# Optimization experiments

Measured on AMD Instinct MI355X. Metric: run time of the kernel, lower is better.

Reference implementation:

```python
import jax, jax.numpy as jnp
import numpy as np

N_NODES = 10000
N_EDGES = 320000
IN_DIM = 256
OUT_DIM = 256
N_REL = 16


def setup_inputs() -> dict:
    key = jax.random.key(0)
    k_x, k_src, k_dst, k_et, k_wr, k_w0 = jax.random.split(key, 6)
    x = jax.random.normal(k_x, (N_NODES, IN_DIM), dtype=jnp.float32)
    src = jax.random.randint(k_src, (N_EDGES,), 0, N_NODES)
    dst = jax.random.randint(k_dst, (N_EDGES,), 0, N_NODES)
    edge_index = jnp.stack([src, dst], axis=0)  # [2, E]
    edge_type = jax.random.randint(k_et, (N_EDGES,), 0, N_REL)
    # Xavier-uniform-ish init for weights
    lim_r = float(np.sqrt(6.0 / (IN_DIM + OUT_DIM)))
    W_r = jax.random.uniform(k_wr, (N_REL, IN_DIM, OUT_DIM), minval=-lim_r, maxval=lim_r, dtype=jnp.float32)
    W0_w = jax.random.uniform(k_w0, (OUT_DIM, IN_DIM), minval=-lim_r, maxval=lim_r, dtype=jnp.float32)
    W0_b = jnp.zeros((OUT_DIM,), dtype=jnp.float32)
    return {
        "x": x,
        "W_r": W_r,
        "W0_w": W0_w,
        "W0_b": W0_b,
        "edge_index": edge_index,
        "edge_type": edge_type,
        "num_nodes_local": N_NODES,
    }


def reference(x, W_r, W0_w, W0_b, edge_index, edge_type, num_nodes_local):
    N = num_nodes_local
    R = W_r.shape[0]
    src = edge_index[0]
    dst = edge_index[1]
    # Per-(relation, dst-node) in-degree, clamped at 1 (matches deg_r.clamp_min(1))
    deg = jnp.zeros((R, N), dtype=x.dtype).at[edge_type, dst].add(1.0)
    deg = jnp.maximum(deg, 1.0)  # [R, N]
    # Transform all nodes under every relation weight: grouped GEMM [R, N, out]
    h_all = jnp.einsum('nd,rdo->rno', x, W_r)
    # Gather per-edge message and normalize by relation-specific dst degree
    msg = h_all[edge_type, src] / deg[edge_type, dst][:, None]  # [E, out]
    # Scatter-add messages to destination nodes
    agg = jax.ops.segment_sum(msg, dst, num_segments=N)  # [N, out]
    # Self-loop transform W_0(x)
    return agg + x @ W0_w.T + W0_b
```

## Files before the change

### kernel.cpp

```cpp
#include <hip/hip_runtime.h>

typedef __bf16 bf16x8 __attribute__((ext_vector_type(8)));
typedef float f32x4 __attribute__((ext_vector_type(4)));

static __device__ __forceinline__ unsigned short f2bf(float f) {
    union { float f; unsigned int u; } v; v.f = f;
    unsigned int r = v.u + 0x7fffu + ((v.u >> 16) & 1u);
    return (unsigned short)(r >> 16);
}
static __device__ __forceinline__ float blo(unsigned int u) {
    union { unsigned int u; float f; } v; v.u = u << 16; return v.f;
}
static __device__ __forceinline__ float bhi(unsigned int u) {
    union { unsigned int u; float f; } v; v.u = u & 0xffff0000u; return v.f;
}
static __device__ __forceinline__ unsigned int pack2(float a, float b) {
    return (unsigned int)f2bf(a) | ((unsigned int)f2bf(b) << 16);
}

__global__ void zero_kernel(int* __restrict__ p, int n) {
    int i = blockIdx.x * blockDim.x + threadIdx.x;
    int n4 = n >> 2;
    if (i < n4) reinterpret_cast<int4*>(p)[i] = make_int4(0, 0, 0, 0);
    if (i < (n & 3)) p[(n4 << 2) + i] = 0;
}

__global__ void prep_kernel(const int* __restrict__ dst, const int* __restrict__ et,
                            int* __restrict__ deg,
                            const float* __restrict__ Wr, const float* __restrict__ W0w,
                            unsigned short* __restrict__ Wt2,
                            const float* __restrict__ x, unsigned short* __restrict__ s,
                            int E, int N, int R, int nh, int nw) {
    const int bid = blockIdx.x, tid = threadIdx.x;
    const int K = (R + 1) * 256;
    if (bid < nh) {
        int i = bid * 256 + tid;
        if (i < E) atomicAdd(&deg[et[i] * N + dst[i]], 1);
    } else if (bid < nh + nw) {
        int t = bid - nh;
        int o = t / (R + 1), kb = t - o * (R + 1);
        float v = (kb < R) ? Wr[(((size_t)kb << 8) + tid) * 256 + o]
                           : W0w[((size_t)o << 8) + tid];
        Wt2[(size_t)o * K + (kb << 8) + tid] = f2bf(v);
    } else {
        int id = (bid - nh - nw) * 256 + tid;
        int n = id >> 6, c4 = id & 63;
        if (n < N) {
            float4 v = *reinterpret_cast<const float4*>(&x[((size_t)n << 8) + (c4 << 2)]);
            ushort4 h;
            h.x = f2bf(v.x); h.y = f2bf(v.y); h.z = f2bf(v.z); h.w = f2bf(v.w);
            *reinterpret_cast<ushort4*>(&s[(size_t)n * K + (K - 256) + (c4 << 2)]) = h;
        }
    }
}

__global__ void scan1_kernel(const int* __restrict__ deg, int* __restrict__ local,
                             int* __restrict__ bsum, int* __restrict__ ctr, int B) {
    __shared__ int tmp[256];
    int t = threadIdx.x, g = blockIdx.x * 256 + t;
    int v = (g < B) ? deg[g] : 0;
    tmp[t] = v; __syncthreads();
    for (int o = 1; o < 256; o <<= 1) {
        int u = (t >= o) ? tmp[t - o] : 0;
        __syncthreads();
        tmp[t] += u;
        __syncthreads();
    }
    if (g < B) { local[g] = tmp[t] - v; ctr[g] = 0; }
    if (t == 255) bsum[blockIdx.x] = tmp[t];
}

__global__ void scan2_kernel(const int* __restrict__ bsum, int* __restrict__ base, int nc) {
    __shared__ int tmp[1024];
    int t = threadIdx.x;
    int v = (t < nc) ? bsum[t] : 0;
    tmp[t] = v; __syncthreads();
    for (int o = 1; o < 1024; o <<= 1) {
        int u = (t >= o) ? tmp[t - o] : 0;
        __syncthreads();
        tmp[t] += u;
        __syncthreads();
    }
    if (t < nc) base[t] = tmp[t] - v;
}

__global__ void scatter_ids_kernel(const int* __restrict__ src, const int* __restrict__ dst,
                                   const int* __restrict__ et, const int* __restrict__ local,
                                   const int* __restrict__ base, int* __restrict__ ctr,
                                   int* __restrict__ srcs, int E, int N) {
    int i = blockIdx.x * blockDim.x + threadIdx.x;
    if (i < E) {
        int b = et[i] * N + dst[i];
        int p = local[b] + base[b >> 8] + atomicAdd(&ctr[b], 1);
        srcs[p] = src[i];
    }
}

__global__ __launch_bounds__(256) void reduce_kernel(
    const int* __restrict__ srcs, const int* __restrict__ deg,
    const int* __restrict__ local, const int* __restrict__ base,
    unsigned short* __restrict__ s, int N, int R)
{
    const int K = (R + 1) * 256;
    const int r = blockIdx.y;
    const int dn = blockIdx.x * 8 + (threadIdx.x >> 5);
    if (dn >= N) return;
    const int lane = threadIdx.x & 31;
    const int bin = r * N + dn;
    const int cnt = deg[bin];
    const int st  = local[bin] + base[bin >> 8];

    float a0 = 0.f, a1 = 0.f, a2 = 0.f, a3 = 0.f;
    float a4 = 0.f, a5 = 0.f, a6 = 0.f, a7 = 0.f;
    for (int c0 = 0; c0 < cnt; c0 += 32) {
        int sv = 0;
        if (c0 + lane < cnt) sv = srcs[st + c0 + lane];
        int m = cnt - c0; if (m > 32) m = 32;
        for (int i = 0; i < m; ++i) {
            int sn = __shfl(sv, i, 32);
            const uint4 v = *reinterpret_cast<const uint4*>(
                &s[(size_t)sn * K + (K - 256) + (lane << 3)]);
            a0 += blo(v.x); a1 += bhi(v.x);
            a2 += blo(v.y); a3 += bhi(v.y);
            a4 += blo(v.z); a5 += bhi(v.z);
            a6 += blo(v.w); a7 += bhi(v.w);
        }
    }
    if (cnt > 0) {
        float sc = 1.0f / (float)cnt;
        a0 *= sc; a1 *= sc; a2 *= sc; a3 *= sc;
        a4 *= sc; a5 *= sc; a6 *= sc; a7 *= sc;
    }
    uint4 o;
    o.x = pack2(a0, a1); o.y = pack2(a2, a3);
    o.z = pack2(a4, a5); o.w = pack2(a6, a7);
    *reinterpret_cast<uint4*>(&s[(size_t)dn * K + (r << 8) + (lane << 3)]) = o;
}

__global__ __launch_bounds__(256) void gemm_kernel(
    const unsigned short* __restrict__ S, const unsigned short* __restrict__ Wt2,
    const float* __restrict__ bias, float* __restrict__ dest,
    int M, int K, int ksteps, int addbias)
{
    __shared__ __align__(16) unsigned short ldsA[2][4096];
    __shared__ __align__(16) unsigned short ldsB[8192];
    const int tid = threadIdx.x;
    const int lane = tid & 63, w = tid >> 6;
    const int wm = w & 1, wn = w >> 1;
    const int m0 = blockIdx.x * 64, n0 = blockIdx.y * 128;
    const int kstart = blockIdx.z * ksteps * 64;
    const size_t rowb = (size_t)K * 2;

    f32x4 acc[2][4] = {};

#define STAGE_A(buf, kstep)                                                               \
    {                                                                                     \
        const int kb = (kstart + (kstep) * 64) * 2;                                       \
        _Pragma("unroll")                                                                 \
        for (int i = 0; i < 2; ++i) {                                                     \
            int flat = (w * 2 + i) * 64 + lane;                                           \
            int row = flat >> 3, seg = flat & 7;                                          \
            int gr = m0 + row; gr = gr < M ? gr : M - 1;                                  \
            const char* gp = (const char*)S + (size_t)gr * rowb + kb                      \
                             + ((seg * 16) ^ ((row & 7) << 4));                           \
            unsigned short* lp = &ldsA[buf][(w * 2 + i) * 512];                           \
            __builtin_amdgcn_global_load_lds(                                             \
                (const __attribute__((address_space(1))) void*)gp,                        \
                (__attribute__((address_space(3))) void*)lp, 16, 0, 0);                   \
        }                                                                                 \
    }

#define STAGE_B(kstep)                                                                    \
    {                                                                                     \
        const int kb = (kstart + (kstep) * 64) * 2;                                       \
        _Pragma("unroll")                                                                 \
        for (int i = 0; i < 4; ++i) {                                                     \
            int flat = (w * 4 + i) * 64 + lane;                                           \
            int row = flat >> 3, seg = flat & 7;                                          \
            const char* gp = (const char*)Wt2 + (size_t)(n0 + row) * rowb + kb            \
                             + ((seg * 16) ^ ((row & 7) << 4));                           \
            unsigned short* lp = &ldsB[(w * 4 + i) * 512];                                \
            __builtin_amdgcn_global_load_lds(                                             \
                (const __attribute__((address_space(1))) void*)gp,                        \
                (__attribute__((address_space(3))) void*)lp, 16, 0, 0);                   \
        }                                                                                 \
    }

#define COMPUTE(buf)                                                                      \
    {                                                                                     \
        _Pragma("unroll")                                                                 \
        for (int kk = 0; kk < 2; ++kk) {                                                  \
            bf16x8 af[2], bfr[4];                                                         \
            _Pragma("unroll")                                                             \
            for (int m = 0; m < 2; ++m) {                                                 \
                int row = wm * 32 + m * 16 + (lane & 15);                                 \
                int colb = (kk * 64 + ((lane >> 4) << 4)) ^ ((row & 7) << 4);             \
                af[m] = *reinterpret_cast<const bf16x8*>(                                 \
                    (const char*)&ldsA[buf][0] + row * 128 + colb);                       \
            }                                                                             \
            _Pragma("unroll")                                                             \
            for (int n = 0; n < 4; ++n) {                                                 \
                int row = wn * 64 + n * 16 + (lane & 15);                                 \
                int colb = (kk * 64 + ((lane >> 4) << 4)) ^ ((row & 7) << 4);             \
                bfr[n] = *reinterpret_cast<const bf16x8*>(                                \
                    (const char*)&ldsB[0] + row * 128 + colb);                            \
            }                                                                             \
            __builtin_amdgcn_s_setprio(1);                                                \
            _Pragma("unroll")                                                             \
            for (int m = 0; m < 2; ++m)                                                   \
                _Pragma("unroll")                                                         \
                for (int n = 0; n < 4; ++n)                                               \
                    acc[m][n] = __builtin_amdgcn_mfma_f32_16x16x32_bf16(                  \
                        af[m], bfr[n], acc[m][n], 0, 0, 0);                               \
            __builtin_amdgcn_s_setprio(0);                                                \
        }                                                                                 \
    }

    STAGE_A(0, 0)
    STAGE_B(0)
    STAGE_A(1, 1)
    asm volatile("s_waitcnt vmcnt(2)" ::: "memory");
    __builtin_amdgcn_s_barrier();

    for (int t = 0; t < ksteps; ++t) {
        COMPUTE(t & 1)
        asm volatile("s_waitcnt lgkmcnt(0)" ::: "memory");
        __builtin_amdgcn_sched_barrier(0);
        __builtin_amdgcn_s_barrier();
        if (t + 1 < ksteps) {
            STAGE_B(t + 1)
            if (t + 2 < ksteps) {
                STAGE_A(t & 1, t + 2)
                asm volatile("s_waitcnt vmcnt(2)" ::: "memory");
            } else {
                asm volatile("s_waitcnt vmcnt(0)" ::: "memory");
            }
            __builtin_amdgcn_s_barrier();
        }
    }
#undef STAGE_A
#undef STAGE_B
#undef COMPUTE

    float* dst = dest + (size_t)blockIdx.z * M * 256;
    const int rbase = m0 + wm * 32 + ((lane >> 4) << 2);
    const int cbase = n0 + wn * 64 + (lane & 15);
    #pragma unroll
    for (int n = 0; n < 4; ++n) {
        int c = cbase + n * 16;
        float bv = addbias ? bias[c] : 0.0f;
        #pragma unroll
        for (int m = 0; m < 2; ++m) {
            #pragma unroll
            for (int j = 0; j < 4; ++j) {
                int r = rbase + m * 16 + j;
                if (r < M) dst[(size_t)r * 256 + c] = acc[m][n][j] + bv;
            }
        }
    }
}

__global__ void combine_kernel(const float* __restrict__ pbuf, const float* __restrict__ bias,
                               float* __restrict__ out, int M, int KZ) {
    int id = blockIdx.x * blockDim.x + threadIdx.x;
    if (id >= M * 64) return;
    int n = id >> 6, c4 = id & 63;
    float4 a = *reinterpret_cast<const float4*>(&pbuf[((size_t)n << 8) + (c4 << 2)]);
    for (int kz = 1; kz < KZ; ++kz) {
        float4 b = *reinterpret_cast<const float4*>(&pbuf[(size_t)kz * M * 256 + ((size_t)n << 8) + (c4 << 2)]);
        a.x += b.x; a.y += b.y; a.z += b.z; a.w += b.w;
    }
    const float4 bv = *reinterpret_cast<const float4*>(&bias[c4 << 2]);
    a.x += bv.x; a.y += bv.y; a.z += bv.z; a.w += bv.w;
    *reinterpret_cast<float4*>(&out[((size_t)n << 8) + (c4 << 2)]) = a;
}

extern "C" void kernel_launch(void* const* d_in, const int* in_sizes, int n_in,
                              void* d_out, int out_size, void* d_ws, size_t ws_size,
                              hipStream_t stream) {
    const float* x   = (const float*)d_in[0];
    const float* Wr  = (const float*)d_in[1];
    const float* W0w = (const float*)d_in[2];
    const float* W0b = (const float*)d_in[3];
    const int*   eidx= (const int*)d_in[4];
    const int*   et  = (const int*)d_in[5];
    const int N = in_sizes[0] / 256;
    const int R = in_sizes[1] / 65536;
    const int E = in_sizes[5];
    const int* src = eidx;
    const int* dst = eidx + E;
    float* out = (float*)d_out;

    const int B = R * N;
    const int NC = (B + 255) / 256;
    const int K = (R + 1) * 256;

    const size_t sz_pslice = (size_t)N * 256 * 4;
    const size_t sz_sort = (((size_t)B * 4 + 255) & ~255UL) * 3
                         + (((size_t)E * 4 + 255) & ~255UL)
                         + 2 * 4096;
    const size_t sz_wt2 = (size_t)256 * K * 2;
    const size_t sz_s   = (size_t)N * K * 2;
    int KZ = 1;
    for (int kz = 4; kz >= 1; kz >>= 1) {
        size_t r0 = (kz > 1) ? (size_t)kz * sz_pslice : 0;
        if (sz_sort > r0) r0 = sz_sort;
        size_t need = ((r0 + 255) & ~255UL) + ((sz_wt2 + 255) & ~255UL) + sz_s + 1024;
        if (need <= ws_size || kz == 1) { KZ = kz; break; }
    }

    char* ws = (char*)d_ws;
    size_t off = 0;
    auto alloc = [&](size_t bytes) { void* p = ws + off; off = (off + bytes + 255) & ~(size_t)255; return p; };
    float* pbuf = (float*)ws;
    int* deg    = (int*)alloc((size_t)B * 4);
    int* local  = (int*)alloc((size_t)B * 4);
    int* bsum   = (int*)alloc(4096);
    int* base   = (int*)alloc(4096);
    int* ctr    = (int*)alloc((size_t)B * 4);
    int* srcs   = (int*)alloc((size_t)E * 4);
    size_t region0 = (KZ > 1) ? (size_t)KZ * sz_pslice : 0;
    if (off > region0) region0 = off;
    off = (region0 + 255) & ~(size_t)255;
    unsigned short* Wt2 = (unsigned short*)alloc(sz_wt2);
    unsigned short* s   = (unsigned short*)alloc(sz_s);

    zero_kernel<<<(B / 4 + 255) / 256, 256, 0, stream>>>(deg, B);
    {
        const int nh = (E + 255) / 256;
        const int nw = (R + 1) * 256;
        const int nx = (N * 64 + 255) / 256;
        prep_kernel<<<nh + nw + nx, 256, 0, stream>>>(dst, et, deg, Wr, W0w, Wt2, x, s,
                                                      E, N, R, nh, nw);
    }
    scan1_kernel<<<NC, 256, 0, stream>>>(deg, local, bsum, ctr, B);
    scan2_kernel<<<1, 1024, 0, stream>>>(bsum, base, NC);
    scatter_ids_kernel<<<(E + 255) / 256, 256, 0, stream>>>(src, dst, et, local, base, ctr, srcs, E, N);
    {
        dim3 g((N + 7) / 8, R);
        reduce_kernel<<<g, 256, 0, stream>>>(srcs, deg, local, base, s, N, R);
    }
    {
        const int ktot = K / 64;
        const int ksteps = ktot / KZ;
        dim3 grid((N + 63) / 64, 2, KZ);
        if (KZ == 1) {
            gemm_kernel<<<grid, 256, 0, stream>>>(s, Wt2, W0b, out, N, K, ksteps, 1);
        } else {
            gemm_kernel<<<grid, 256, 0, stream>>>(s, Wt2, W0b, pbuf, N, K, ksteps, 0);
            combine_kernel<<<(N * 64 + 255) / 256, 256, 0, stream>>>(pbuf, W0b, out, N, KZ);
        }
    }
}
```

Baseline: 141.8 us.

## Fuse per-relation gather-mean into GEMM A-tile staging with fixed 4-way K split

Replaces the separate reduce kernel, which wrote mean-aggregated bf16 rows into a large [N, (R+1)*256] buffer, with a fused kernel. That kernel gathers neighbor features per relation straight into LDS and runs the MFMA GEMM over that relation's 256-wide K slice. A 64x256 output tile per block is accumulated across a fixed split of relations into four partial buffers, which a combine kernel then sums. This removes the round trip of the big intermediate through global memory. In exchange, each block serializes its gather latency before the MFMA work, and the workspace-size check is dropped in favor of always allocating four partial slices.

```diff
diff --git a/kernel.cpp b/kernel.cpp
--- a/kernel.cpp
+++ b/kernel.cpp
@@ -29,7 +29,7 @@
                             int* __restrict__ deg,
                             const float* __restrict__ Wr, const float* __restrict__ W0w,
                             unsigned short* __restrict__ Wt2,
-                            const float* __restrict__ x, unsigned short* __restrict__ s,
+                            const float* __restrict__ x, unsigned short* __restrict__ xbf,
                             int E, int N, int R, int nh, int nw) {
     const int bid = blockIdx.x, tid = threadIdx.x;
     const int K = (R + 1) * 256;
@@ -49,7 +49,7 @@
             float4 v = *reinterpret_cast<const float4*>(&x[((size_t)n << 8) + (c4 << 2)]);
             ushort4 h;
             h.x = f2bf(v.x); h.y = f2bf(v.y); h.z = f2bf(v.z); h.w = f2bf(v.w);
-            *reinterpret_cast<ushort4*>(&s[(size_t)n * K + (K - 256) + (c4 << 2)]) = h;
+            *reinterpret_cast<ushort4*>(&xbf[((size_t)n << 8) + (c4 << 2)]) = h;
         }
     }
 }
@@ -96,165 +96,139 @@
     }
 }
 
-__global__ __launch_bounds__(256) void reduce_kernel(
-    const int* __restrict__ srcs, const int* __restrict__ deg,
-    const int* __restrict__ local, const int* __restrict__ base,
-    unsigned short* __restrict__ s, int N, int R)
+__global__ __launch_bounds__(256) void fused_kernel(
+    const unsigned short* __restrict__ xbf, const unsigned short* __restrict__ Wt2,
+    const int* __restrict__ deg, const int* __restrict__ local,
+    const int* __restrict__ basep, const int* __restrict__ srcs,
+    float* __restrict__ pbuf, int M, int R, int K)
 {
-    const int K = (R + 1) * 256;
-    const int r = blockIdx.y;
-    const int dn = blockIdx.x * 8 + (threadIdx.x >> 5);
-    if (dn >= N) return;
-    const int lane = threadIdx.x & 31;
-    const int bin = r * N + dn;
-    const int cnt = deg[bin];
-    const int st  = local[bin] + base[bin >> 8];
-
-    float a0 = 0.f, a1 = 0.f, a2 = 0.f, a3 = 0.f;
-    float a4 = 0.f, a5 = 0.f, a6 = 0.f, a7 = 0.f;
-    for (int c0 = 0; c0 < cnt; c0 += 32) {
-        int sv = 0;
-        if (c0 + lane < cnt) sv = srcs[st + c0 + lane];
-        int m = cnt - c0; if (m > 32) m = 32;
-        for (int i = 0; i < m; ++i) {
-            int sn = __shfl(sv, i, 32);
-            const uint4 v = *reinterpret_cast<const uint4*>(
-                &s[(size_t)sn * K + (K - 256) + (lane << 3)]);
-            a0 += blo(v.x); a1 += bhi(v.x);
-            a2 += blo(v.y); a3 += bhi(v.y);
-            a4 += blo(v.z); a5 += bhi(v.z);
-            a6 += blo(v.w); a7 += bhi(v.w);
-        }
-    }
-    if (cnt > 0) {
-        float sc = 1.0f / (float)cnt;
-        a0 *= sc; a1 *= sc; a2 *= sc; a3 *= sc;
-        a4 *= sc; a5 *= sc; a6 *= sc; a7 *= sc;
-    }
-    uint4 o;
-    o.x = pack2(a0, a1); o.y = pack2(a2, a3);
-    o.z = pack2(a4, a5); o.w = pack2(a6, a7);
-    *reinterpret_cast<uint4*>(&s[(size_t)dn * K + (r << 8) + (lane << 3)]) = o;
-}
-
-__global__ __launch_bounds__(256) void gemm_kernel(
-    const unsigned short* __restrict__ S, const unsigned short* __restrict__ Wt2,
-    const float* __restrict__ bias, float* __restrict__ dest,
-    int M, int K, int ksteps, int addbias)
-{
-    __shared__ __align__(16) unsigned short ldsA[2][4096];
-    __shared__ __align__(16) unsigned short ldsB[8192];
+    __shared__ __align__(16) unsigned short ldsA[64 * 256];
+    __shared__ __align__(16) unsigned short ldsB[2][256 * 32];
     const int tid = threadIdx.x;
     const int lane = tid & 63, w = tid >> 6;
-    const int wm = w & 1, wn = w >> 1;
-    const int m0 = blockIdx.x * 64, n0 = blockIdx.y * 128;
-    const int kstart = blockIdx.z * ksteps * 64;
-    const size_t rowb = (size_t)K * 2;
-
-    f32x4 acc[2][4] = {};
-
-#define STAGE_A(buf, kstep)                                                               \
+    const int hw = tid >> 5, l = tid & 31;
+    const int m0 = blockIdx.x * 64;
+    const int z = blockIdx.y;
+    const int sl0 = (z * (R + 1)) >> 2, sl1 = ((z + 1) * (R + 1)) >> 2;
+    const size_t rowbW = (size_t)K * 2;
+
+    f32x4 acc[4][4] = {};
+
+#define STAGE_B(buf, sl, ks)                                                              \
     {                                                                                     \
-        const int kb = (kstart + (kstep) * 64) * 2;                                       \
+        const size_t kb = ((size_t)(sl) * 256 + (size_t)(ks) * 32) * 2;                   \
         _Pragma("unroll")                                                                 \
-        for (int i = 0; i < 2; ++i) {                                                     \
-            int flat = (w * 2 + i) * 64 + lane;                                           \
-            int row = flat >> 3, seg = flat & 7;                                          \
-            int gr = m0 + row; gr = gr < M ? gr : M - 1;                                  \
-            const char* gp = (const char*)S + (size_t)gr * rowb + kb                      \
-                             + ((seg * 16) ^ ((row & 7) << 4));                           \
-            unsigned short* lp = &ldsA[buf][(w * 2 + i) * 512];                           \
+        for (int i = 0; i < 4; ++i) {                                                     \
+            int flat = i * 256 + tid;                                                     \
+            int rowq = flat >> 2, seg = flat & 3;                                         \
+            const char* gp = (const char*)Wt2 + (size_t)rowq * rowbW + kb                 \
+                             + ((seg << 4) ^ ((rowq & 3) << 4));                          \
+            unsigned short* lp = &ldsB[buf][flat << 3];                                   \
             __builtin_amdgcn_global_load_lds(                                             \
                 (const __attribute__((address_space(1))) void*)gp,                        \
                 (__attribute__((address_space(3))) void*)lp, 16, 0, 0);                   \
         }                                                                                 \
     }
 
-#define STAGE_B(kstep)                                                                    \
+#define COMPUTE(buf, ks)                                                                  \
     {                                                                                     \
-        const int kb = (kstart + (kstep) * 64) * 2;                                       \
+        bf16x8 af[4], bfr[4];                                                             \
         _Pragma("unroll")                                                                 \
-        for (int i = 0; i < 4; ++i) {                                                     \
-            int flat = (w * 4 + i) * 64 + lane;                                           \
-            int row = flat >> 3, seg = flat & 7;                                          \
-            const char* gp = (const char*)Wt2 + (size_t)(n0 + row) * rowb + kb            \
-                             + ((seg * 16) ^ ((row & 7) << 4));                           \
-            unsigned short* lp = &ldsB[(w * 4 + i) * 512];                                \
-            __builtin_amdgcn_global_load_lds(                                             \
-                (const __attribute__((address_space(1))) void*)gp,                        \
-                (__attribute__((address_space(3))) void*)lp, 16, 0, 0);                   \
+        for (int mi = 0; mi < 4; ++mi) {                                                  \
+            int row = mi * 16 + (lane & 15);                                              \
+            int colb = ((ks) * 64 + ((lane >> 4) << 4)) ^ ((row & 7) << 4);               \
+            af[mi] = *reinterpret_cast<const bf16x8*>((const char*)ldsA + row * 512 + colb); \
         }                                                                                 \
-    }
-
-#define COMPUTE(buf)                                                                      \
-    {                                                                                     \
         _Pragma("unroll")                                                                 \
-        for (int kk = 0; kk < 2; ++kk) {                                                  \
-            bf16x8 af[2], bfr[4];                                                         \
+        for (int ni = 0; ni < 4; ++ni) {                                                  \
+            int row = w * 64 + ni * 16 + (lane & 15);                                     \
+            int colb = (((lane >> 4) << 4)) ^ ((row & 3) << 4);                           \
+            bfr[ni] = *reinterpret_cast<const bf16x8*>((const char*)&ldsB[buf][0] + row * 64 + colb); \
+        }                                                                                 \
+        __builtin_amdgcn_s_setprio(1);                                                    \
+        _Pragma("unroll")                                                                 \
+        for (int mi = 0; mi < 4; ++mi)                                                    \
             _Pragma("unroll")                                                             \
-            for (int m = 0; m < 2; ++m) {                                                 \
-                int row = wm * 32 + m * 16 + (lane & 15);                                 \
-                int colb = (kk * 64 + ((lane >> 4) << 4)) ^ ((row & 7) << 4);             \
-                af[m] = *reinterpret_cast<const bf16x8*>(                                 \
-                    (const char*)&ldsA[buf][0] + row * 128 + colb);                       \
-            }                                                                             \
-            _Pragma("unroll")                                                             \
-            for (int n = 0; n < 4; ++n) {                                                 \
-                int row = wn * 64 + n * 16 + (lane & 15);                                 \
-                int colb = (kk * 64 + ((lane >> 4) << 4)) ^ ((row & 7) << 4);             \
-                bfr[n] = *reinterpret_cast<const bf16x8*>(                                \
-                    (const char*)&ldsB[0] + row * 128 + colb);                            \
-            }                                                                             \
-            __builtin_amdgcn_s_setprio(1);                                                \
-            _Pragma("unroll")                                                             \
-            for (int m = 0; m < 2; ++m)                                                   \
-                _Pragma("unroll")                                                         \
-                for (int n = 0; n < 4; ++n)                                               \
-                    acc[m][n] = __builtin_amdgcn_mfma_f32_16x16x32_bf16(                  \
-                        af[m], bfr[n], acc[m][n], 0, 0, 0);                               \
-            __builtin_amdgcn_s_setprio(0);                                                \
-        }                                                                                 \
-    }
-
-    STAGE_A(0, 0)
-    STAGE_B(0)
-    STAGE_A(1, 1)
-    asm volatile("s_waitcnt vmcnt(2)" ::: "memory");
-    __builtin_amdgcn_s_barrier();
-
-    for (int t = 0; t < ksteps; ++t) {
-        COMPUTE(t & 1)
-        asm volatile("s_waitcnt lgkmcnt(0)" ::: "memory");
+            for (int ni = 0; ni < 4; ++ni)                                                \
+                acc[mi][ni] = __builtin_amdgcn_mfma_f32_16x16x32_bf16(                    \
+                    af[mi], bfr[ni], acc[mi][ni], 0, 0, 0);                               \
+        __builtin_amdgcn_s_setprio(0);                                                    \
+    }
+
+    for (int sl = sl0; sl < sl1; ++sl) {
+        STAGE_B(0, sl, 0)
+        if (sl == R) {
+            #pragma unroll
+            for (int j = 0; j < 8; ++j) {
+                int row = hw * 8 + j;
+                int dn = m0 + row;
+                uint4 v = make_uint4(0, 0, 0, 0);
+                if (dn < M) v = *reinterpret_cast<const uint4*>(&xbf[((size_t)dn << 8) + (l << 3)]);
+                *reinterpret_cast<uint4*>((char*)ldsA + row * 512 + (((l << 4)) ^ ((row & 7) << 4))) = v;
+            }
+        } else {
+            for (int j = 0; j < 8; ++j) {
+                int row = hw * 8 + j;
+                int dn = m0 + row;
+                float a0 = 0.f, a1 = 0.f, a2 = 0.f, a3 = 0.f;
+                float a4 = 0.f, a5 = 0.f, a6 = 0.f, a7 = 0.f;
+                if (dn < M) {
+                    int bin = sl * M + dn;
+                    int cnt = deg[bin];
+                    if (cnt > 0) {
+                        int st = local[bin] + basep[bin >> 8];
+                        for (int c0 = 0; c0 < cnt; c0 += 32) {
+                            int sv = (c0 + l < cnt) ? srcs[st + c0 + l] : 0;
+                            int mm = cnt - c0; if (mm > 32) mm = 32;
+                            for (int i = 0; i < mm; ++i) {
+                                int sn = __shfl(sv, i, 32);
+                                const uint4 v = *reinterpret_cast<const uint4*>(
+                                    &xbf[((size_t)sn << 8) + (l << 3)]);
+                                a0 += blo(v.x); a1 += bhi(v.x);
+                                a2 += blo(v.y); a3 += bhi(v.y);
+                                a4 += blo(v.z); a5 += bhi(v.z);
+                                a6 += blo(v.w); a7 += bhi(v.w);
+                            }
+                        }
+                        float sc = 1.0f / (float)cnt;
+                        a0 *= sc; a1 *= sc; a2 *= sc; a3 *= sc;
+                        a4 *= sc; a5 *= sc; a6 *= sc; a7 *= sc;
+                    }
+                }
+                uint4 o;
+                o.x = pack2(a0, a1); o.y = pack2(a2, a3);
+                o.z = pack2(a4, a5); o.w = pack2(a6, a7);
+                *reinterpret_cast<uint4*>((char*)ldsA + row * 512 + (((l << 4)) ^ ((row & 7) << 4))) = o;
+            }
+        }
+        asm volatile("s_waitcnt vmcnt(0) lgkmcnt(0)" ::: "memory");
         __builtin_amdgcn_sched_barrier(0);
         __builtin_amdgcn_s_barrier();
-        if (t + 1 < ksteps) {
-            STAGE_B(t + 1)
-            if (t + 2 < ksteps) {
-                STAGE_A(t & 1, t + 2)
-                asm volatile("s_waitcnt vmcnt(2)" ::: "memory");
+        for (int ks = 0; ks < 8; ++ks) {
+            if (ks < 7) {
+                STAGE_B((ks + 1) & 1, sl, ks + 1)
+                asm volatile("s_waitcnt vmcnt(4)" ::: "memory");
             } else {
                 asm volatile("s_waitcnt vmcnt(0)" ::: "memory");
             }
             __builtin_amdgcn_s_barrier();
+            COMPUTE(ks & 1, ks)
+            __builtin_amdgcn_s_barrier();
         }
     }
-#undef STAGE_A
 #undef STAGE_B
 #undef COMPUTE
 
-    float* dst = dest + (size_t)blockIdx.z * M * 256;
-    const int rbase = m0 + wm * 32 + ((lane >> 4) << 2);
-    const int cbase = n0 + wn * 64 + (lane & 15);
+    float* dp = pbuf + (size_t)z * M * 256;
     #pragma unroll
-    for (int n = 0; n < 4; ++n) {
-        int c = cbase + n * 16;
-        float bv = addbias ? bias[c] : 0.0f;
+    for (int ni = 0; ni < 4; ++ni) {
+        int c = w * 64 + ni * 16 + (lane & 15);
         #pragma unroll
-        for (int m = 0; m < 2; ++m) {
+        for (int mi = 0; mi < 4; ++mi) {
             #pragma unroll
             for (int j = 0; j < 4; ++j) {
-                int r = rbase + m * 16 + j;
-                if (r < M) dst[(size_t)r * 256 + c] = acc[m][n][j] + bv;
+                int r = m0 + mi * 16 + ((lane >> 4) << 2) + j;
+                if (r < M) dp[(size_t)r * 256 + c] = acc[mi][ni][j];
             }
         }
     }
@@ -295,60 +269,34 @@
     const int NC = (B + 255) / 256;
     const int K = (R + 1) * 256;
 
-    const size_t sz_pslice = (size_t)N * 256 * 4;
-    const size_t sz_sort = (((size_t)B * 4 + 255) & ~255UL) * 3
-                         + (((size_t)E * 4 + 255) & ~255UL)
-                         + 2 * 4096;
-    const size_t sz_wt2 = (size_t)256 * K * 2;
-    const size_t sz_s   = (size_t)N * K * 2;
-    int KZ = 1;
-    for (int kz = 4; kz >= 1; kz >>= 1) {
-        size_t r0 = (kz > 1) ? (size_t)kz * sz_pslice : 0;
-        if (sz_sort > r0) r0 = sz_sort;
-        size_t need = ((r0 + 255) & ~255UL) + ((sz_wt2 + 255) & ~255UL) + sz_s + 1024;
-        if (need <= ws_size || kz == 1) { KZ = kz; break; }
-    }
-
     char* ws = (char*)d_ws;
     size_t off = 0;
     auto alloc = [&](size_t bytes) { void* p = ws + off; off = (off + bytes + 255) & ~(size_t)255; return p; };
-    float* pbuf = (float*)ws;
     int* deg    = (int*)alloc((size_t)B * 4);
     int* local  = (int*)alloc((size_t)B * 4);
     int* bsum   = (int*)alloc(4096);
     int* base   = (int*)alloc(4096);
     int* ctr    = (int*)alloc((size_t)B * 4);
     int* srcs   = (int*)alloc((size_t)E * 4);
-    size_t region0 = (KZ > 1) ? (size_t)KZ * sz_pslice : 0;
-    if (off > region0) region0 = off;
-    off = (region0 + 255) & ~(size_t)255;
-    unsigned short* Wt2 = (unsigned short*)alloc(sz_wt2);
-    unsigned short* s   = (unsigned short*)alloc(sz_s);
+    unsigned short* xbf = (unsigned short*)alloc((size_t)N * 256 * 2);
+    unsigned short* Wt2 = (unsigned short*)alloc((size_t)256 * K * 2);
+    float* pbuf = (float*)alloc((size_t)4 * N * 256 * 4);
+    (void)ws_size;
 
     zero_kernel<<<(B / 4 + 255) / 256, 256, 0, stream>>>(deg, B);
     {
         const int nh = (E + 255) / 256;
         const int nw = (R + 1) * 256;
         const int nx = (N * 64 + 255) / 256;
-        prep_kernel<<<nh + nw + nx, 256, 0, stream>>>(dst, et, deg, Wr, W0w, Wt2, x, s,
+        prep_kernel<<<nh + nw + nx, 256, 0, stream>>>(dst, et, deg, Wr, W0w, Wt2, x, xbf,
                                                       E, N, R, nh, nw);
     }
     scan1_kernel<<<NC, 256, 0, stream>>>(deg, local, bsum, ctr, B);
     scan2_kernel<<<1, 1024, 0, stream>>>(bsum, base, NC);
     scatter_ids_kernel<<<(E + 255) / 256, 256, 0, stream>>>(src, dst, et, local, base, ctr, srcs, E, N);
     {
-        dim3 g((N + 7) / 8, R);
-        reduce_kernel<<<g, 256, 0, stream>>>(srcs, deg, local, base, s, N, R);
-    }
-    {
-        const int ktot = K / 64;
-        const int ksteps = ktot / KZ;
-        dim3 grid((N + 63) / 64, 2, KZ);
-        if (KZ == 1) {
-            gemm_kernel<<<grid, 256, 0, stream>>>(s, Wt2, W0b, out, N, K, ksteps, 1);
-        } else {
-            gemm_kernel<<<grid, 256, 0, stream>>>(s, Wt2, W0b, pbuf, N, K, ksteps, 0);
-            combine_kernel<<<(N * 64 + 255) / 256, 256, 0, stream>>>(pbuf, W0b, out, N, KZ);
-        }
-    }
-}
+        dim3 grid((N + 63) / 64, 4);
+        fused_kernel<<<grid, 256, 0, stream>>>(xbf, Wt2, deg, local, base, srcs, pbuf, N, R, K);
+    }
+    combine_kernel<<<(N * 64 + 255) / 256, 256, 0, stream>>>(pbuf, W0b, out, N, 4);
+}
```

After: 208.5 us. 47.1% more time.
